# Kernel tuning notes

Measured on AMD Instinct MI355X. Metric: run time of the kernel, lower is better.

The kernel has to match this reference:

```python
import jax, jax.numpy as jnp
import numpy as np

LN_EPS = 1e-5

def layernorm(x, w, b):
    # LayerNorm over last dim (head_dim), affine
    mu = jnp.mean(x, axis=-1, keepdims=True)
    var = jnp.mean(jnp.square(x - mu), axis=-1, keepdims=True)
    return (x - mu) * jax.lax.rsqrt(var + LN_EPS) * w + b

def setup_inputs() -> dict:
    key = jax.random.key(0)
    ks = jax.random.split(key, 6)
    B, N, C, H = 2, 2048, 1024, 16
    hd = C // H
    s = 1.0 / np.sqrt(C)
    return {
        "x": jax.random.normal(ks[0], (B, N, C), jnp.float32),
        "W_qkv": jax.random.normal(ks[1], (C, 3 * C), jnp.float32) * s,  # qkv_bias=False
        "qn_w": jnp.ones((hd,), jnp.float32),
        "qn_b": jnp.zeros((hd,), jnp.float32),
        "kn_w": jnp.ones((hd,), jnp.float32),
        "kn_b": jnp.zeros((hd,), jnp.float32),
        "W_proj": jax.random.normal(ks[2], (C, C), jnp.float32) * s,
        "b_proj": jnp.zeros((C,), jnp.float32),
    }

def reference(x, W_qkv, qn_w, qn_b, kn_w, kn_b, W_proj, b_proj):
    B, N, C = x.shape
    H = 16
    hd = C // H
    scale = hd ** -0.5
    qkv = (x @ W_qkv).reshape(B, N, 3, H, hd)
    qkv = jnp.transpose(qkv, (2, 0, 3, 1, 4))  # [3,B,H,N,hd]
    q, k, v = qkv[0], qkv[1], qkv[2]
    q = layernorm(q, qn_w, qn_b)
    k = layernorm(k, kn_w, kn_b)
    q = q * scale
    attn = jnp.einsum('bhnd,bhmd->bhnm', q, k)  # [B,H,N,N]
    attn = jax.nn.softmax(attn, axis=-1)  # attn_drop p=0 -> identity
    o = jnp.einsum('bhnm,bhmd->bhnd', attn, v)
    o = jnp.transpose(o, (0, 2, 1, 3)).reshape(B, N, C)
    return o @ W_proj + b_proj  # proj_drop p=0 -> identity
```

## Files before the change

### kernel.cpp

```cpp
#include <hip/hip_runtime.h>
#include <hip/hip_bf16.h>

#define B_  2
#define N_  2048
#define C_  1024
#define H_  16
#define HD_ 64
#define QSZ (B_*N_*C_)
#define QSCALE 0.18033688011112042f

typedef __attribute__((ext_vector_type(8))) short short8;
typedef __attribute__((ext_vector_type(4))) float floatx4;
typedef __attribute__((ext_vector_type(4))) unsigned short ushort4v;

__device__ __forceinline__ unsigned short f2bf(float f) {
    unsigned int u = __builtin_bit_cast(unsigned int, f);
    u += 0x7fff + ((u >> 16) & 1);
    return (unsigned short)(u >> 16);
}
__device__ __forceinline__ float bf2f(unsigned short h) {
    return __builtin_bit_cast(float, (unsigned int)h << 16);
}
__device__ __forceinline__ unsigned int pk2bf(float a, float b) {
    unsigned int ua = __builtin_bit_cast(unsigned int, a);
    unsigned int ub = __builtin_bit_cast(unsigned int, b);
    ua += 0x7fff + ((ua >> 16) & 1);
    ub += 0x7fff + ((ub >> 16) & 1);
    return __builtin_amdgcn_perm(ub, ua, 0x07060302);
}

__device__ __forceinline__ void g2l16(const void* g, void* l) {
    __builtin_amdgcn_global_load_lds(
        (const __attribute__((address_space(1))) void*)g,
        (__attribute__((address_space(3))) void*)l, 16, 0, 0);
}

__global__ __launch_bounds__(256) void pack_bf16_kernel(
    const float* __restrict__ src, unsigned short* __restrict__ dst)
{
    const int i = blockIdx.x * 256 + threadIdx.x;
    float4 v = ((const float4*)src)[i];
    ushort4 o = {f2bf(v.x), f2bf(v.y), f2bf(v.z), f2bf(v.w)};
    ((ushort4*)dst)[i] = o;
}

__global__ __launch_bounds__(256) void transpose_pack2_kernel(
    const float* __restrict__ Wq, unsigned short* __restrict__ Wqt,
    const float* __restrict__ Wp, unsigned short* __restrict__ Wpt)
{
    __shared__ unsigned short tl[32][34];
    const bool isq = blockIdx.x < 96;
    const int bx = isq ? blockIdx.x : blockIdx.x - 96;
    const int Nd = isq ? 3072 : 1024;
    const float* W = isq ? Wq : Wp;
    unsigned short* Wt = isq ? Wqt : Wpt;
    const int r  = threadIdx.x >> 3;
    const int c4 = (threadIdx.x & 7) * 4;
    const int n0 = bx * 32, k0 = blockIdx.y * 32;
    float4 v = *(const float4*)&W[(size_t)(k0 + r) * Nd + n0 + c4];
    tl[r][c4 + 0] = f2bf(v.x); tl[r][c4 + 1] = f2bf(v.y);
    tl[r][c4 + 2] = f2bf(v.z); tl[r][c4 + 3] = f2bf(v.w);
    __syncthreads();
    ushort4 o = {tl[c4 + 0][r], tl[c4 + 1][r], tl[c4 + 2][r], tl[c4 + 3][r]};
    *(ushort4*)&Wt[(size_t)(n0 + r) * 1024 + k0 + c4] = o;
}

#define GEMM_CORE(A_, Bt_, Kd_, row0_, col0_)                                 \
    __shared__ unsigned short As[128 * 32];                                   \
    __shared__ unsigned short Bs[128 * 32];                                   \
    const int t    = threadIdx.x;                                             \
    const int lane = t & 63;                                                  \
    const int w    = t >> 6;                                                  \
    const int l15  = lane & 15;                                               \
    const int quad = lane >> 4;                                               \
    const int wm   = w >> 1, wn = w & 1;                                      \
    size_t aOff = (size_t)(row0_ + w * 16 + (lane >> 2)) * Kd_ + (lane & 3) * 8; \
    size_t bOff = (size_t)(col0_ + w * 16 + (lane >> 2)) * Kd_ + (lane & 3) * 8; \
    floatx4 acc[4][4];                                                        \
    _Pragma("unroll")                                                         \
    for (int i = 0; i < 4; ++i)                                               \
        _Pragma("unroll")                                                     \
        for (int j = 0; j < 4; ++j) acc[i][j] = floatx4{0.f, 0.f, 0.f, 0.f};  \
    for (int k0 = 0; k0 < Kd_; k0 += 32) {                                    \
        _Pragma("unroll")                                                     \
        for (int c = 0; c < 2; ++c) {                                         \
            g2l16(&A_[aOff + (size_t)c * 64 * Kd_ + k0],                      \
                  &As[(w * 16 + c * 64) * 32]);                               \
            g2l16(&Bt_[bOff + (size_t)c * 64 * Kd_ + k0],                     \
                  &Bs[(w * 16 + c * 64) * 32]);                               \
        }                                                                     \
        __syncthreads();                                                      \
        short8 af[4], bf[4];                                                  \
        _Pragma("unroll")                                                     \
        for (int i = 0; i < 4; ++i)                                           \
            af[i] = *(const short8*)&As[(wm * 64 + i * 16 + l15) * 32 + quad * 8]; \
        _Pragma("unroll")                                                     \
        for (int j = 0; j < 4; ++j)                                           \
            bf[j] = *(const short8*)&Bs[(wn * 64 + j * 16 + l15) * 32 + quad * 8]; \
        _Pragma("unroll")                                                     \
        for (int i = 0; i < 4; ++i)                                           \
            _Pragma("unroll")                                                 \
            for (int j = 0; j < 4; ++j)                                       \
                acc[i][j] = __builtin_amdgcn_mfma_f32_16x16x32_bf16(          \
                    af[i], bf[j], acc[i][j], 0, 0, 0);                        \
        __syncthreads();                                                      \
    }

__global__ __launch_bounds__(256) void gemm_qkv_kernel(
    const unsigned short* __restrict__ X,
    const unsigned short* __restrict__ Wt,
    const float* __restrict__ qn_w, const float* __restrict__ qn_b,
    const float* __restrict__ kn_w, const float* __restrict__ kn_b,
    unsigned short* __restrict__ qb, unsigned short* __restrict__ kb,
    unsigned short* __restrict__ vb)
{
    const int row0 = blockIdx.y * 128;
    const int col0 = blockIdx.x * 128;
    GEMM_CORE(X, Wt, 1024, row0, col0)
    const int which = col0 >> 10;
    const int h = ((col0 & 1023) >> 6) + wn;
    if (which == 2) {
        #pragma unroll
        for (int j = 0; j < 4; ++j) {
            const int d = j * 16 + l15;
            #pragma unroll
            for (int i = 0; i < 4; ++i) {
                #pragma unroll
                for (int r = 0; r < 4; ++r) {
                    const int grow = row0 + wm * 64 + i * 16 + quad * 4 + r;
                    const int bidx = grow >> 11, n = grow & 2047;
                    vb[(((size_t)(bidx * H_ + h) * N_ + n) * HD_) + d] =
                        f2bf(acc[i][j][r]);
                }
            }
        }
    } else {
        const float* wt = (which == 0) ? qn_w : kn_w;
        const float* bi = (which == 0) ? qn_b : kn_b;
        unsigned short* dstbuf = (which == 0) ? qb : kb;
        float w4[4], b4[4];
        #pragma unroll
        for (int j = 0; j < 4; ++j) {
            w4[j] = wt[j * 16 + l15];
            b4[j] = bi[j * 16 + l15];
        }
        #pragma unroll
        for (int i = 0; i < 4; ++i) {
            #pragma unroll
            for (int r = 0; r < 4; ++r) {
                float v0 = acc[i][0][r], v1 = acc[i][1][r],
                      v2 = acc[i][2][r], v3 = acc[i][3][r];
                float s = (v0 + v1) + (v2 + v3);
                #pragma unroll
                for (int o = 1; o < 16; o <<= 1) s += __shfl_xor(s, o);
                const float mu = s * (1.0f / 64.0f);
                const float d0 = v0 - mu, d1 = v1 - mu,
                            d2 = v2 - mu, d3 = v3 - mu;
                float s2 = (d0 * d0 + d1 * d1) + (d2 * d2 + d3 * d3);
                #pragma unroll
                for (int o = 1; o < 16; o <<= 1) s2 += __shfl_xor(s2, o);
                const float rstd = rsqrtf(s2 * (1.0f / 64.0f) + 1e-5f);
                float y0 = d0 * rstd * w4[0] + b4[0];
                float y1 = d1 * rstd * w4[1] + b4[1];
                float y2 = d2 * rstd * w4[2] + b4[2];
                float y3 = d3 * rstd * w4[3] + b4[3];
                if (which == 0) {
                    y0 *= QSCALE; y1 *= QSCALE; y2 *= QSCALE; y3 *= QSCALE;
                }
                const int grow = row0 + wm * 64 + i * 16 + quad * 4 + r;
                const int bidx = grow >> 11, n = grow & 2047;
                unsigned short* dp =
                    &dstbuf[(((size_t)(bidx * H_ + h) * N_ + n) * HD_) + l15];
                dp[0]  = f2bf(y0);
                dp[16] = f2bf(y1);
                dp[32] = f2bf(y2);
                dp[48] = f2bf(y3);
            }
        }
    }
}

__global__ __launch_bounds__(256) void gemm_proj_kernel(
    const unsigned short* __restrict__ O,
    const unsigned short* __restrict__ Wt,
    const float* __restrict__ bias, float* __restrict__ out)
{
    __shared__ unsigned short As[64 * 32];
    __shared__ unsigned short Bs[128 * 32];
    const int t    = threadIdx.x;
    const int lane = t & 63;
    const int w    = t >> 6;
    const int l15  = lane & 15;
    const int quad = lane >> 4;
    const int row0 = blockIdx.y * 64;
    const int col0 = blockIdx.x * 128;
    size_t aOff = (size_t)(row0 + w * 16 + (lane >> 2)) * 1024 + (lane & 3) * 8;
    size_t bOff = (size_t)(col0 + w * 16 + (lane >> 2)) * 1024 + (lane & 3) * 8;
    floatx4 acc[4][2];
    #pragma unroll
    for (int i = 0; i < 4; ++i)
        #pragma unroll
        for (int j = 0; j < 2; ++j) acc[i][j] = floatx4{0.f, 0.f, 0.f, 0.f};
    for (int k0 = 0; k0 < 1024; k0 += 32) {
        g2l16(&O[aOff + k0], &As[(w * 16) * 32]);
        #pragma unroll
        for (int c = 0; c < 2; ++c)
            g2l16(&Wt[bOff + (size_t)c * 64 * 1024 + k0],
                  &Bs[(w * 16 + c * 64) * 32]);
        __syncthreads();
        short8 af[4], bf[2];
        #pragma unroll
        for (int i = 0; i < 4; ++i)
            af[i] = *(const short8*)&As[(i * 16 + l15) * 32 + quad * 8];
        #pragma unroll
        for (int j = 0; j < 2; ++j)
            bf[j] = *(const short8*)&Bs[(w * 32 + j * 16 + l15) * 32 + quad * 8];
        #pragma unroll
        for (int i = 0; i < 4; ++i)
            #pragma unroll
            for (int j = 0; j < 2; ++j)
                acc[i][j] = __builtin_amdgcn_mfma_f32_16x16x32_bf16(
                    af[i], bf[j], acc[i][j], 0, 0, 0);
        __syncthreads();
    }
    #pragma unroll
    for (int j = 0; j < 2; ++j) {
        const int gcol = col0 + w * 32 + j * 16 + l15;
        const float b = bias[gcol];
        #pragma unroll
        for (int i = 0; i < 4; ++i) {
            #pragma unroll
            for (int r = 0; r < 4; ++r) {
                const int grow = row0 + i * 16 + quad * 4 + r;
                out[(size_t)grow * 1024 + gcol] = acc[i][j][r] + b;
            }
        }
    }
}

__global__ __launch_bounds__(256, 2) void flash_kernel(
    const unsigned short* __restrict__ qb, const unsigned short* __restrict__ kb,
    const unsigned short* __restrict__ vb, unsigned short* __restrict__ ob)
{
    __shared__ __align__(16) unsigned short Ks[128 * 72];
    __shared__ __align__(16) unsigned short Vt[64 * 136];
    __shared__ __align__(16) unsigned short Pb[128 * 136];
    const int t    = threadIdx.x;
    const int lane = t & 63;
    const int w    = t >> 6;
    const int l15  = lane & 15;
    const int quad = lane >> 4;
    const int q0   = blockIdx.x * 128;
    const int bh   = blockIdx.y;
    const unsigned short* Q = qb + (size_t)bh * N_ * HD_;
    const unsigned short* K = kb + (size_t)bh * N_ * HD_;
    const unsigned short* V = vb + (size_t)bh * N_ * HD_;

    {
        const int r = t >> 3, c = (t & 7) * 8;
        #pragma unroll
        for (int rep = 0; rep < 4; ++rep)
            *(short8*)&Pb[(rep * 32 + r) * 136 + c] =
                *(const short8*)&Q[(size_t)(q0 + rep * 32 + r) * 64 + c];
    }
    __syncthreads();
    short8 qf[2][2];
    #pragma unroll
    for (int qg = 0; qg < 2; ++qg)
        #pragma unroll
        for (int kk = 0; kk < 2; ++kk)
            qf[qg][kk] = *(const short8*)
                &Pb[(qg * 64 + w * 16 + l15) * 136 + kk * 32 + quad * 8];

    floatx4 acc[2][4];
    #pragma unroll
    for (int qg = 0; qg < 2; ++qg)
        #pragma unroll
        for (int dt = 0; dt < 4; ++dt) acc[qg][dt] = floatx4{0.f, 0.f, 0.f, 0.f};
    float l_part[2] = {0.f, 0.f};

    const int kr = t & 127, kc = (t >> 7) * 32;
    const int vkv = (t & 63) * 2, vd = (t >> 6) * 16;

    short8 kR[4], vR[4];
    #pragma unroll
    for (int c = 0; c < 4; ++c)
        kR[c] = *(const short8*)&K[(size_t)kr * 64 + kc + c * 8];
    vR[0] = *(const short8*)&V[(size_t)vkv * 64 + vd];
    vR[1] = *(const short8*)&V[(size_t)vkv * 64 + vd + 8];
    vR[2] = *(const short8*)&V[(size_t)(vkv + 1) * 64 + vd];
    vR[3] = *(const short8*)&V[(size_t)(vkv + 1) * 64 + vd + 8];

    for (int kt = 0; kt < N_; kt += 128) {
        __syncthreads();
        #pragma unroll
        for (int c = 0; c < 4; ++c)
            *(short8*)&Ks[kr * 72 + kc + c * 8] = kR[c];
        #pragma unroll
        for (int j = 0; j < 8; ++j) {
            unsigned int p0 = (unsigned int)(unsigned short)vR[0][j] |
                              ((unsigned int)(unsigned short)vR[2][j] << 16);
            unsigned int p1 = (unsigned int)(unsigned short)vR[1][j] |
                              ((unsigned int)(unsigned short)vR[3][j] << 16);
            *(unsigned int*)&Vt[(vd + j) * 136 + vkv]     = p0;
            *(unsigned int*)&Vt[(vd + 8 + j) * 136 + vkv] = p1;
        }
        __syncthreads();
        if (kt + 128 < N_) {
            const int kt2 = kt + 128;
            #pragma unroll
            for (int c = 0; c < 4; ++c)
                kR[c] = *(const short8*)&K[(size_t)(kt2 + kr) * 64 + kc + c * 8];
            vR[0] = *(const short8*)&V[(size_t)(kt2 + vkv) * 64 + vd];
            vR[1] = *(const short8*)&V[(size_t)(kt2 + vkv) * 64 + vd + 8];
            vR[2] = *(const short8*)&V[(size_t)(kt2 + vkv + 1) * 64 + vd];
            vR[3] = *(const short8*)&V[(size_t)(kt2 + vkv + 1) * 64 + vd + 8];
        }

        floatx4 sc[2][8];
        #pragma unroll
        for (int ct = 0; ct < 8; ++ct) {
            short8 a0 = *(const short8*)&Ks[(ct * 16 + l15) * 72 + quad * 8];
            short8 a1 = *(const short8*)&Ks[(ct * 16 + l15) * 72 + 32 + quad * 8];
            #pragma unroll
            for (int qg = 0; qg < 2; ++qg) {
                floatx4 r = {0.f, 0.f, 0.f, 0.f};
                r = __builtin_amdgcn_mfma_f32_16x16x32_bf16(a0, qf[qg][0], r, 0, 0, 0);
                r = __builtin_amdgcn_mfma_f32_16x16x32_bf16(a1, qf[qg][1], r, 0, 0, 0);
                sc[qg][ct] = r;
            }
        }

        #pragma unroll
        for (int qg = 0; qg < 2; ++qg) {
            const int prow = qg * 64 + w * 16 + l15;
            #pragma unroll
            for (int ct = 0; ct < 8; ++ct) {
                float p0 = __builtin_amdgcn_exp2f(sc[qg][ct][0]);
                float p1 = __builtin_amdgcn_exp2f(sc[qg][ct][1]);
                float p2 = __builtin_amdgcn_exp2f(sc[qg][ct][2]);
                float p3 = __builtin_amdgcn_exp2f(sc[qg][ct][3]);
                l_part[qg] += (p0 + p1) + (p2 + p3);
                uint2 pk;
                pk.x = pk2bf(p0, p1);
                pk.y = pk2bf(p2, p3);
                *(uint2*)&Pb[prow * 136 + ct * 16 + quad * 4] = pk;
            }
        }
        asm volatile("" ::: "memory");

        #pragma unroll
        for (int kk = 0; kk < 4; ++kk) {
            short8 pbf[2];
            #pragma unroll
            for (int qg = 0; qg < 2; ++qg)
                pbf[qg] = *(const short8*)
                    &Pb[(qg * 64 + w * 16 + l15) * 136 + kk * 32 + quad * 8];
            #pragma unroll
            for (int dt = 0; dt < 4; ++dt) {
                short8 va = *(const short8*)
                    &Vt[(dt * 16 + l15) * 136 + kk * 32 + quad * 8];
                #pragma unroll
                for (int qg = 0; qg < 2; ++qg)
                    acc[qg][dt] = __builtin_amdgcn_mfma_f32_16x16x32_bf16(
                        va, pbf[qg], acc[qg][dt], 0, 0, 0);
            }
        }
    }

    asm volatile("" ::: "memory");
    #pragma unroll
    for (int qg = 0; qg < 2; ++qg) {
        l_part[qg] += __shfl_xor(l_part[qg], 16);
        l_part[qg] += __shfl_xor(l_part[qg], 32);
        const float inv = 1.0f / l_part[qg];
        const int orow = qg * 64 + w * 16 + l15;
        #pragma unroll
        for (int dt = 0; dt < 4; ++dt) {
            uint2 o2;
            o2.x = pk2bf(acc[qg][dt][0] * inv, acc[qg][dt][1] * inv);
            o2.y = pk2bf(acc[qg][dt][2] * inv, acc[qg][dt][3] * inv);
            *(uint2*)&Pb[orow * 136 + dt * 16 + quad * 4] = o2;
        }
    }
    __syncthreads();
    const int bidx = bh >> 4, h = bh & 15;
    {
        const int r = t >> 3, c = (t & 7) * 8;
        #pragma unroll
        for (int rep = 0; rep < 4; ++rep) {
            const int row = rep * 32 + r;
            *(short8*)&ob[((size_t)(bidx * N_ + q0 + row)) * C_ + h * 64 + c] =
                *(const short8*)&Pb[row * 136 + c];
        }
    }
}

extern "C" void kernel_launch(void* const* d_in, const int* in_sizes, int n_in,
                              void* d_out, int out_size, void* d_ws, size_t ws_size,
                              hipStream_t stream) {
    const float* x      = (const float*)d_in[0];
    const float* W_qkv  = (const float*)d_in[1];
    const float* qn_w   = (const float*)d_in[2];
    const float* qn_b   = (const float*)d_in[3];
    const float* kn_w   = (const float*)d_in[4];
    const float* kn_b   = (const float*)d_in[5];
    const float* W_proj = (const float*)d_in[6];
    const float* b_proj = (const float*)d_in[7];
    float* out = (float*)d_out;

    unsigned short* qb  = (unsigned short*)d_ws;
    unsigned short* kb  = qb + (size_t)QSZ;
    unsigned short* vb  = kb + (size_t)QSZ;
    unsigned short* ob  = vb + (size_t)QSZ;
    unsigned short* xb  = ob + (size_t)B_ * N_ * C_;
    unsigned short* wqt = xb + (size_t)B_ * N_ * C_;
    unsigned short* wpt = wqt + (size_t)3 * C_ * C_;

    pack_bf16_kernel<<<dim3((B_ * N_ * C_) / 1024), 256, 0, stream>>>(x, xb);
    transpose_pack2_kernel<<<dim3(128, 32), 256, 0, stream>>>(W_qkv, wqt, W_proj, wpt);
    gemm_qkv_kernel<<<dim3(24, 32), 256, 0, stream>>>(
        xb, wqt, qn_w, qn_b, kn_w, kn_b, qb, kb, vb);
    flash_kernel<<<dim3(N_ / 128, B_ * H_), 256, 0, stream>>>(qb, kb, vb, ob);
    gemm_proj_kernel<<<dim3(8, 64), 256, 0, stream>>>(ob, wpt, b_proj, out);
}
```

Baseline: 202.9 us.

## Split flash attention key tile across warp pairs with split-K reduction

Reassigns work in the flash kernel so each warp covers 64 query rows (four 16-row tiles) and half of each 128-key tile, instead of 16 rows over two groups across all keys. Each K/V fragment loaded from LDS is now reused across four query tiles, which cuts LDS reads per MFMA. The price is an end-of-kernel reduction: the two key halves merge partial accumulators and row sums through fp32 LDS with extra barriers before normalising and writing bf16 output. Accumulator registers double (acc[4][4]), which may put the two-blocks-per-CU occupancy at risk.

```diff
diff --git a/kernel.cpp b/kernel.cpp
--- a/kernel.cpp
+++ b/kernel.cpp
@@ -11,15 +11,11 @@
 
 typedef __attribute__((ext_vector_type(8))) short short8;
 typedef __attribute__((ext_vector_type(4))) float floatx4;
-typedef __attribute__((ext_vector_type(4))) unsigned short ushort4v;
 
 __device__ __forceinline__ unsigned short f2bf(float f) {
     unsigned int u = __builtin_bit_cast(unsigned int, f);
     u += 0x7fff + ((u >> 16) & 1);
     return (unsigned short)(u >> 16);
-}
-__device__ __forceinline__ float bf2f(unsigned short h) {
-    return __builtin_bit_cast(float, (unsigned int)h << 16);
 }
 __device__ __forceinline__ unsigned int pk2bf(float a, float b) {
     unsigned int ua = __builtin_bit_cast(unsigned int, a);
@@ -245,9 +241,12 @@
     __shared__ __align__(16) unsigned short Ks[128 * 72];
     __shared__ __align__(16) unsigned short Vt[64 * 136];
     __shared__ __align__(16) unsigned short Pb[128 * 136];
+    __shared__ float Lb[128];
     const int t    = threadIdx.x;
     const int lane = t & 63;
     const int w    = t >> 6;
+    const int qg   = w & 1;
+    const int kvh  = w >> 1;
     const int l15  = lane & 15;
     const int quad = lane >> 4;
     const int q0   = blockIdx.x * 128;
@@ -264,20 +263,20 @@
                 *(const short8*)&Q[(size_t)(q0 + rep * 32 + r) * 64 + c];
     }
     __syncthreads();
-    short8 qf[2][2];
-    #pragma unroll
-    for (int qg = 0; qg < 2; ++qg)
+    short8 qf[4][2];
+    #pragma unroll
+    for (int qt = 0; qt < 4; ++qt)
         #pragma unroll
         for (int kk = 0; kk < 2; ++kk)
-            qf[qg][kk] = *(const short8*)
-                &Pb[(qg * 64 + w * 16 + l15) * 136 + kk * 32 + quad * 8];
-
-    floatx4 acc[2][4];
-    #pragma unroll
-    for (int qg = 0; qg < 2; ++qg)
-        #pragma unroll
-        for (int dt = 0; dt < 4; ++dt) acc[qg][dt] = floatx4{0.f, 0.f, 0.f, 0.f};
-    float l_part[2] = {0.f, 0.f};
+            qf[qt][kk] = *(const short8*)
+                &Pb[(qg * 64 + qt * 16 + l15) * 136 + kk * 32 + quad * 8];
+
+    floatx4 acc[4][4];
+    #pragma unroll
+    for (int qt = 0; qt < 4; ++qt)
+        #pragma unroll
+        for (int dt = 0; dt < 4; ++dt) acc[qt][dt] = floatx4{0.f, 0.f, 0.f, 0.f};
+    float l_part[4] = {0.f, 0.f, 0.f, 0.f};
 
     const int kr = t & 127, kc = (t >> 7) * 32;
     const int vkv = (t & 63) * 2, vd = (t >> 6) * 16;
@@ -317,81 +316,98 @@
             vR[3] = *(const short8*)&V[(size_t)(kt2 + vkv + 1) * 64 + vd + 8];
         }
 
-        floatx4 sc[2][8];
-        #pragma unroll
-        for (int ct = 0; ct < 8; ++ct) {
+        #pragma unroll
+        for (int ci = 0; ci < 4; ++ci) {
+            const int ct = kvh * 4 + ci;
             short8 a0 = *(const short8*)&Ks[(ct * 16 + l15) * 72 + quad * 8];
             short8 a1 = *(const short8*)&Ks[(ct * 16 + l15) * 72 + 32 + quad * 8];
             #pragma unroll
-            for (int qg = 0; qg < 2; ++qg) {
-                floatx4 r = {0.f, 0.f, 0.f, 0.f};
-                r = __builtin_amdgcn_mfma_f32_16x16x32_bf16(a0, qf[qg][0], r, 0, 0, 0);
-                r = __builtin_amdgcn_mfma_f32_16x16x32_bf16(a1, qf[qg][1], r, 0, 0, 0);
-                sc[qg][ct] = r;
-            }
-        }
-
-        #pragma unroll
-        for (int qg = 0; qg < 2; ++qg) {
-            const int prow = qg * 64 + w * 16 + l15;
-            #pragma unroll
-            for (int ct = 0; ct < 8; ++ct) {
-                float p0 = __builtin_amdgcn_exp2f(sc[qg][ct][0]);
-                float p1 = __builtin_amdgcn_exp2f(sc[qg][ct][1]);
-                float p2 = __builtin_amdgcn_exp2f(sc[qg][ct][2]);
-                float p3 = __builtin_amdgcn_exp2f(sc[qg][ct][3]);
-                l_part[qg] += (p0 + p1) + (p2 + p3);
+            for (int qt = 0; qt < 4; ++qt) {
+                floatx4 s = {0.f, 0.f, 0.f, 0.f};
+                s = __builtin_amdgcn_mfma_f32_16x16x32_bf16(a0, qf[qt][0], s, 0, 0, 0);
+                s = __builtin_amdgcn_mfma_f32_16x16x32_bf16(a1, qf[qt][1], s, 0, 0, 0);
+                const float p0 = __builtin_amdgcn_exp2f(s[0]);
+                const float p1 = __builtin_amdgcn_exp2f(s[1]);
+                const float p2 = __builtin_amdgcn_exp2f(s[2]);
+                const float p3 = __builtin_amdgcn_exp2f(s[3]);
+                l_part[qt] += (p0 + p1) + (p2 + p3);
                 uint2 pk;
                 pk.x = pk2bf(p0, p1);
                 pk.y = pk2bf(p2, p3);
-                *(uint2*)&Pb[prow * 136 + ct * 16 + quad * 4] = pk;
+                *(uint2*)&Pb[(qg * 64 + qt * 16 + l15) * 136 + ct * 16 + quad * 4] = pk;
             }
         }
         asm volatile("" ::: "memory");
 
         #pragma unroll
-        for (int kk = 0; kk < 4; ++kk) {
-            short8 pbf[2];
-            #pragma unroll
-            for (int qg = 0; qg < 2; ++qg)
-                pbf[qg] = *(const short8*)
-                    &Pb[(qg * 64 + w * 16 + l15) * 136 + kk * 32 + quad * 8];
+        for (int kk2 = 0; kk2 < 2; ++kk2) {
+            const int kk = kvh * 2 + kk2;
+            short8 pbf[4];
+            #pragma unroll
+            for (int qt = 0; qt < 4; ++qt)
+                pbf[qt] = *(const short8*)
+                    &Pb[(qg * 64 + qt * 16 + l15) * 136 + kk * 32 + quad * 8];
             #pragma unroll
             for (int dt = 0; dt < 4; ++dt) {
                 short8 va = *(const short8*)
                     &Vt[(dt * 16 + l15) * 136 + kk * 32 + quad * 8];
                 #pragma unroll
-                for (int qg = 0; qg < 2; ++qg)
-                    acc[qg][dt] = __builtin_amdgcn_mfma_f32_16x16x32_bf16(
-                        va, pbf[qg], acc[qg][dt], 0, 0, 0);
+                for (int qt = 0; qt < 4; ++qt)
+                    acc[qt][dt] = __builtin_amdgcn_mfma_f32_16x16x32_bf16(
+                        va, pbf[qt], acc[qt][dt], 0, 0, 0);
             }
         }
     }
 
-    asm volatile("" ::: "memory");
-    #pragma unroll
-    for (int qg = 0; qg < 2; ++qg) {
-        l_part[qg] += __shfl_xor(l_part[qg], 16);
-        l_part[qg] += __shfl_xor(l_part[qg], 32);
-        const float inv = 1.0f / l_part[qg];
-        const int orow = qg * 64 + w * 16 + l15;
-        #pragma unroll
-        for (int dt = 0; dt < 4; ++dt) {
-            uint2 o2;
-            o2.x = pk2bf(acc[qg][dt][0] * inv, acc[qg][dt][1] * inv);
-            o2.y = pk2bf(acc[qg][dt][2] * inv, acc[qg][dt][3] * inv);
-            *(uint2*)&Pb[orow * 136 + dt * 16 + quad * 4] = o2;
-        }
+    #pragma unroll
+    for (int qt = 0; qt < 4; ++qt) {
+        l_part[qt] += __shfl_xor(l_part[qt], 16);
+        l_part[qt] += __shfl_xor(l_part[qt], 32);
     }
     __syncthreads();
-    const int bidx = bh >> 4, h = bh & 15;
+    float* Pf = (float*)Pb;
+    if (kvh == 0) {
+        #pragma unroll
+        for (int qt = 0; qt < 4; ++qt) {
+            const int q = qg * 64 + qt * 16 + l15;
+            #pragma unroll
+            for (int dt = 0; dt < 4; ++dt)
+                #pragma unroll
+                for (int r = 0; r < 4; ++r)
+                    Pf[q * 68 + dt * 16 + quad * 4 + r] = acc[qt][dt][r];
+            if (quad == 0) Lb[q] = l_part[qt];
+        }
+    }
+    __syncthreads();
+    if (kvh == 1) {
+        #pragma unroll
+        for (int qt = 0; qt < 4; ++qt) {
+            const int q = qg * 64 + qt * 16 + l15;
+            #pragma unroll
+            for (int dt = 0; dt < 4; ++dt)
+                #pragma unroll
+                for (int r = 0; r < 4; ++r)
+                    Pf[q * 68 + dt * 16 + quad * 4 + r] += acc[qt][dt][r];
+            if (quad == 0) Lb[q] += l_part[qt];
+        }
+    }
+    __syncthreads();
     {
-        const int r = t >> 3, c = (t & 7) * 8;
-        #pragma unroll
-        for (int rep = 0; rep < 4; ++rep) {
-            const int row = rep * 32 + r;
-            *(short8*)&ob[((size_t)(bidx * N_ + q0 + row)) * C_ + h * 64 + c] =
-                *(const short8*)&Pb[row * 136 + c];
+        const int orow = t >> 1, oc = (t & 1) * 32;
+        const float inv = 1.0f / Lb[orow];
+        const int bidx = bh >> 4, h = bh & 15;
+        unsigned short* dst =
+            &ob[((size_t)(bidx * N_ + q0 + orow)) * C_ + h * 64 + oc];
+        #pragma unroll
+        for (int k = 0; k < 4; ++k) {
+            float4 f0 = *(float4*)&Pf[orow * 68 + oc + k * 8];
+            float4 f1 = *(float4*)&Pf[orow * 68 + oc + k * 8 + 4];
+            uint4 u;
+            u.x = pk2bf(f0.x * inv, f0.y * inv);
+            u.y = pk2bf(f0.z * inv, f0.w * inv);
+            u.z = pk2bf(f1.x * inv, f1.y * inv);
+            u.w = pk2bf(f1.z * inv, f1.w * inv);
+            *(uint4*)&dst[k * 8] = u;
         }
     }
 }
```

Measured after the change: 202.1 us. No clear change (-0.4%).
